# Kernel optimization log

Hardware: AMD Instinct MI355X
Metric: run time of the kernel (lower is better)

## Reference

```python
import jax, jax.numpy as jnp
import numpy as np

N_NODES = 200000
N_EDGES = 6400000
N_LAYERS = 3
Z_DIM = 4  # 2*4 + 1 + 3 == 12 == Linear in_features


def setup_inputs() -> dict:
    key = jax.random.key(0)
    ks = jax.random.split(key, 7)
    z = jax.random.normal(ks[0], (N_NODES, Z_DIM), dtype=jnp.float32)
    r = jax.random.uniform(ks[1], (N_EDGES, 1), dtype=jnp.float32)
    r_hat = jax.random.normal(ks[2], (N_EDGES, 3), dtype=jnp.float32)
    # Per-layer Linear(12, 1) weights and biases, stacked over layers.
    W = jax.random.normal(ks[3], (N_LAYERS, 1, 12), dtype=jnp.float32) * (1.0 / np.sqrt(12.0))
    b = jnp.zeros((N_LAYERS, 1), dtype=jnp.float32)
    src = jax.random.randint(ks[4], (N_EDGES,), 0, N_NODES, dtype=jnp.int32)
    dst = jax.random.randint(ks[5], (N_EDGES,), 0, N_NODES, dtype=jnp.int32)
    return {"z": z, "r": r, "r_hat": r_hat, "W": W, "b": b, "src": src, "dst": dst}


def reference(z, r, r_hat, W, b, src, dst):
    # batch['x'] = batch['z'].copy()
    x = z
    n_nodes = z.shape[0]
    for i in range(W.shape[0]):
        # Per-edge gather + concat -> [E, 12]
        inpt = jnp.concatenate([z[src], z[dst], r, r_hat], axis=-1)
        # Tiny Linear(12, 1) -> per-edge scalar message [E, 1]
        msg = inpt @ W[i].T + b[i]
        # Scatter-sum messages onto destination nodes, residual update.
        agg = jax.ops.segment_sum(msg, dst, num_segments=n_nodes)  # [N, 1]
        z = z + agg  # broadcast over the 4 node features
    return z, x
```

## Files before the change

### kernel.cpp

```cpp
#include <hip/hip_runtime.h>

#define N_NODES 200000
#define N_EDGES 6400000
#define K_BUCKETS 256
#define BUCKET 784
#define NSB 3200
#define CHUNK 2000
#define P_SPLIT 8

__device__ __forceinline__ unsigned short f2bf(float x) {
    unsigned u = __float_as_uint(x);
    u += 0x7fffu + ((u >> 16) & 1u);
    return (unsigned short)(u >> 16);
}
__device__ __forceinline__ float bf2f(unsigned short h) {
    return __uint_as_float((unsigned)h << 16);
}


__global__ __launch_bounds__(256) void prep_kernel(
    const float4* __restrict__ z, float4* __restrict__ x_out,
    const float* __restrict__ W,
    float* __restrict__ u, float* __restrict__ v)
{
    int n = blockIdx.x * 256 + threadIdx.x;
    if (n >= N_NODES) return;
    float4 zv = z[n];
    x_out[n] = zv;
    float a0 = W[0], a1 = W[1], a2 = W[2], a3 = W[3];
    float q0 = W[4], q1 = W[5], q2 = W[6], q3 = W[7];
    u[n] = a0 * zv.x + a1 * zv.y + a2 * zv.z + a3 * zv.w;
    v[n] = q0 * zv.x + q1 * zv.y + q2 * zv.z + q3 * zv.w;
}

__global__ __launch_bounds__(256) void hist_kernel(const int* __restrict__ dst,
                                                   int* __restrict__ counts)
{
    __shared__ int cnt[K_BUCKETS];
    int tid = threadIdx.x, sb = blockIdx.x;
    cnt[tid] = 0;
    __syncthreads();
    int e0 = sb * CHUNK;
    for (int i = tid; i < CHUNK; i += 256)
        atomicAdd(&cnt[dst[e0 + i] / BUCKET], 1);
    __syncthreads();
    counts[sb * K_BUCKETS + tid] = cnt[tid];
}

__global__ __launch_bounds__(256) void scan_cols(const int* __restrict__ counts,
                                                 int* __restrict__ baseRel,
                                                 int* __restrict__ tot)
{
    __shared__ int buf[256];
    __shared__ int carry_s;
    int k = blockIdx.x, tid = threadIdx.x;
    if (tid == 0) carry_s = 0;
    __syncthreads();
    for (int base = 0; base < NSB; base += 256) {
        int idx = base + tid;
        int v = (idx < NSB) ? counts[idx * K_BUCKETS + k] : 0;
        buf[tid] = v;
        __syncthreads();
        for (int off = 1; off < 256; off <<= 1) {
            int t = (tid >= off) ? buf[tid - off] : 0;
            __syncthreads();
            buf[tid] += t;
            __syncthreads();
        }
        int incl = buf[tid];
        if (idx < NSB) baseRel[idx * K_BUCKETS + k] = carry_s + incl - v;
        __syncthreads();
        if (tid == 255) carry_s += incl;
        __syncthreads();
    }
    if (tid == 255) tot[k] = carry_s;
}

__global__ __launch_bounds__(256) void scan_tot(const int* __restrict__ tot,
                                                int* __restrict__ bstart)
{
    __shared__ int buf[256];
    int tid = threadIdx.x;
    int v = tot[tid];
    buf[tid] = v;
    __syncthreads();
    for (int off = 1; off < 256; off <<= 1) {
        int t = (tid >= off) ? buf[tid - off] : 0;
        __syncthreads();
        buf[tid] += t;
        __syncthreads();
    }
    bstart[tid] = buf[tid] - v;
    if (tid == 255) bstart[256] = buf[255];
}

__global__ __launch_bounds__(256) void scatter_kernel(
    const int* __restrict__ src, const int* __restrict__ dst,
    const float* __restrict__ r, const float* __restrict__ r_hat,
    const float* __restrict__ W, const float* __restrict__ b,
    const int* __restrict__ counts, const int* __restrict__ baseRel,
    const int* __restrict__ bstart,
    int* __restrict__ packedA, unsigned* __restrict__ c01a,
    unsigned short* __restrict__ c2a)
{
    __shared__ int cur[K_BUCKETS];
    __shared__ int delta[K_BUCKETS];
    __shared__ int scanbuf[256];
    __shared__ int            lpack[CHUNK];
    __shared__ unsigned       lc01[CHUNK];
    __shared__ unsigned short lc2[CHUNK];
    __shared__ unsigned char  skb[CHUNK];

    int tid = threadIdx.x, sb = blockIdx.x;

    int v = counts[sb * K_BUCKETS + tid];
    scanbuf[tid] = v;
    __syncthreads();
    for (int off = 1; off < 256; off <<= 1) {
        int t = (tid >= off) ? scanbuf[tid - off] : 0;
        __syncthreads();
        scanbuf[tid] += t;
        __syncthreads();
    }
    int localBase = scanbuf[tid] - v;
    int gBase = bstart[tid] + baseRel[sb * K_BUCKETS + tid];
    delta[tid] = gBase - localBase;
    cur[tid] = localBase;
    __syncthreads();

    float w8_0 = W[8],  w9_0 = W[9],  w10_0 = W[10], w11_0 = W[11], b0 = b[0];
    float w8_1 = W[20], w9_1 = W[21], w10_1 = W[22], w11_1 = W[23], b1 = b[1];
    float w8_2 = W[32], w9_2 = W[33], w10_2 = W[34], w11_2 = W[35], b2 = b[2];

    int e0 = sb * CHUNK;
    for (int i = tid; i < CHUNK; i += 256) {
        int e = e0 + i;
        int d = dst[e];
        int k = d / BUCKET;
        int dl = d - k * BUCKET;
        int slot = atomicAdd(&cur[k], 1);
        int sn = src[e];
        float rv = r[e];
        size_t he = 3 * (size_t)e;
        float h0 = r_hat[he], h1 = r_hat[he + 1], h2 = r_hat[he + 2];
        lpack[slot] = (sn << 10) | dl;
        unsigned cc0 = f2bf(w8_0 * rv + w9_0 * h0 + w10_0 * h1 + w11_0 * h2 + b0);
        unsigned cc1 = f2bf(w8_1 * rv + w9_1 * h0 + w10_1 * h1 + w11_1 * h2 + b1);
        lc01[slot] = cc0 | (cc1 << 16);
        lc2[slot]  = f2bf(w8_2 * rv + w9_2 * h0 + w10_2 * h1 + w11_2 * h2 + b2);
        skb[slot]  = (unsigned char)k;
    }
    __syncthreads();

    for (int s = tid; s < CHUNK; s += 256) {
        int k = skb[s];
        int gpos = delta[k] + s;
        packedA[gpos] = lpack[s];
        c01a[gpos] = lc01[s];
        c2a[gpos]  = lc2[s];
    }
}

__global__ __launch_bounds__(256) void pagg_kernel(
    const int* __restrict__ packedA, const unsigned* __restrict__ c01a,
    const unsigned short* __restrict__ c2a, const int* __restrict__ bstart,
    const float* __restrict__ u, const float* __restrict__ v,
    int layer, float* __restrict__ partial)
{
    __shared__ float vsl[BUCKET];
    __shared__ float aggsl[BUCKET];
    int tid = threadIdx.x, blk = blockIdx.x;
    int k = blk / P_SPLIT;
    int p = blk - k * P_SPLIT;
    int nbase = k * BUCKET;
    int nn = min(BUCKET, N_NODES - nbase);

    for (int i = tid; i < BUCKET; i += 256) {
        aggsl[i] = 0.0f;
        vsl[i] = (i < nn) ? v[nbase + i] : 0.0f;
    }
    __syncthreads();

    int estart = bstart[k], eend = bstart[k + 1];
    int len = eend - estart;
    int per = (len + P_SPLIT - 1) / P_SPLIT;
    int lo = estart + p * per;
    int hi = min(lo + per, eend);

    for (int j = lo + tid; j < hi; j += 256) {
        int pack = packedA[j];
        int s = pack >> 10;
        int dl = pack & 1023;
        float c = (layer == 2) ? bf2f(c2a[j])
                               : bf2f((unsigned short)(c01a[j] >> (16 * layer)));
        atomicAdd(&aggsl[dl], u[s] + vsl[dl] + c);
    }
    __syncthreads();

    float* pout = partial + (size_t)blk * BUCKET;
    for (int i = tid; i < BUCKET; i += 256) pout[i] = aggsl[i];
}

__global__ __launch_bounds__(256) void fin_kernel(
    const float4* __restrict__ z0, const float* __restrict__ partial,
    const float* __restrict__ Sin, float* __restrict__ Sout,
    const float* __restrict__ W, int layer,
    float* __restrict__ u, float* __restrict__ v, float4* __restrict__ z_out)
{
    int n = blockIdx.x * 256 + threadIdx.x;
    if (n >= N_NODES) return;
    int k = n / BUCKET;
    int i = n - k * BUCKET;
    float agg = 0.0f;
    const float* pk = partial + (size_t)k * P_SPLIT * BUCKET + i;
#pragma unroll
    for (int p = 0; p < P_SPLIT; ++p) agg += pk[(size_t)p * BUCKET];
    float S = ((layer == 0) ? 0.0f : Sin[n]) + agg;
    if (layer < 2) {
        const float* Wn = W + 12 * (layer + 1);
        float a0 = Wn[0], a1 = Wn[1], a2 = Wn[2], a3 = Wn[3];
        float q0 = Wn[4], q1 = Wn[5], q2 = Wn[6], q3 = Wn[7];
        float A = a0 + a1 + a2 + a3, B = q0 + q1 + q2 + q3;
        float4 zv = z0[n];
        Sout[n] = S;
        u[n] = a0 * zv.x + a1 * zv.y + a2 * zv.z + a3 * zv.w + A * S;
        v[n] = q0 * zv.x + q1 * zv.y + q2 * zv.z + q3 * zv.w + B * S;
    } else {
        float4 zv = z0[n];
        zv.x += S; zv.y += S; zv.z += S; zv.w += S;
        z_out[n] = zv;
    }
}


__global__ __launch_bounds__(256) void init_kernel(
    const float4* __restrict__ z_in, float4* __restrict__ z_cur,
    float4* __restrict__ x_out, float* __restrict__ agg)
{
    int n = blockIdx.x * blockDim.x + threadIdx.x;
    if (n < N_NODES) {
        float4 vv = z_in[n];
        z_cur[n] = vv; x_out[n] = vv; agg[n] = 0.0f;
    }
}

__global__ __launch_bounds__(256) void edge_kernel(
    const float* __restrict__ z, const float* __restrict__ r,
    const float* __restrict__ r_hat, const int* __restrict__ src,
    const int* __restrict__ dst, const float* __restrict__ Wl,
    const float* __restrict__ bl, float* __restrict__ agg)
{
    int e = blockIdx.x * blockDim.x + threadIdx.x;
    if (e >= N_EDGES) return;
    float w0 = Wl[0], w1 = Wl[1], w2 = Wl[2], w3 = Wl[3];
    float w4 = Wl[4], w5 = Wl[5], w6 = Wl[6], w7 = Wl[7];
    float w8 = Wl[8], w9 = Wl[9], w10 = Wl[10], w11 = Wl[11];
    float bias = bl[0];
    int s = src[e], d = dst[e];
    float4 zs = ((const float4*)z)[s];
    float4 zd = ((const float4*)z)[d];
    float rv = r[e];
    const float* rh = r_hat + 3 * (size_t)e;
    float msg = w0*zs.x + w1*zs.y + w2*zs.z + w3*zs.w
              + w4*zd.x + w5*zd.y + w6*zd.z + w7*zd.w
              + w8*rv + w9*rh[0] + w10*rh[1] + w11*rh[2] + bias;
    unsafeAtomicAdd(&agg[d], msg);
}

__global__ __launch_bounds__(256) void node_update(float4* __restrict__ z_cur,
                                                   float* __restrict__ agg)
{
    int n = blockIdx.x * blockDim.x + threadIdx.x;
    if (n < N_NODES) {
        float a = agg[n]; float4 vv = z_cur[n];
        vv.x += a; vv.y += a; vv.z += a; vv.w += a;
        z_cur[n] = vv; agg[n] = 0.0f;
    }
}

__global__ __launch_bounds__(256) void final_update(const float4* __restrict__ z_cur,
                                                    const float* __restrict__ agg,
                                                    float4* __restrict__ z_out)
{
    int n = blockIdx.x * blockDim.x + threadIdx.x;
    if (n < N_NODES) {
        float a = agg[n]; float4 vv = z_cur[n];
        vv.x += a; vv.y += a; vv.z += a; vv.w += a;
        z_out[n] = vv;
    }
}


extern "C" void kernel_launch(void* const* d_in, const int* in_sizes, int n_in,
                              void* d_out, int out_size, void* d_ws, size_t ws_size,
                              hipStream_t stream)
{
    const float* z     = (const float*)d_in[0];
    const float* r     = (const float*)d_in[1];
    const float* r_hat = (const float*)d_in[2];
    const float* W     = (const float*)d_in[3];
    const float* b     = (const float*)d_in[4];
    const int*   src   = (const int*)d_in[5];
    const int*   dst   = (const int*)d_in[6];
    float* out = (float*)d_out;

    char* ws = (char*)d_ws;
    size_t off = 0;
    auto alloc = [&](size_t bytes) {
        void* p = ws + off;
        off += (bytes + 15) & ~(size_t)15;
        return p;
    };
    int*            packedA = (int*)alloc((size_t)N_EDGES * 4);
    unsigned*       c01a    = (unsigned*)alloc((size_t)N_EDGES * 4);
    unsigned short* c2a     = (unsigned short*)alloc((size_t)N_EDGES * 2);
    int*            counts  = (int*)alloc((size_t)NSB * K_BUCKETS * 4);
    int*            baseRel = (int*)alloc((size_t)NSB * K_BUCKETS * 4);
    int*            tot     = (int*)alloc((size_t)K_BUCKETS * 4);
    int*            bstart  = (int*)alloc((size_t)(K_BUCKETS + 1) * 4);
    float*          Sa      = (float*)alloc((size_t)N_NODES * 4);
    float*          Sb      = (float*)alloc((size_t)N_NODES * 4);
    float*          ubuf    = (float*)alloc((size_t)N_NODES * 4);
    float*          vbuf    = (float*)alloc((size_t)N_NODES * 4);
    float*          partial = (float*)alloc((size_t)K_BUCKETS * P_SPLIT * BUCKET * 4);
    size_t required = off;

    dim3 nblk((N_NODES + 255) / 256);

    if (ws_size >= required) {
        prep_kernel<<<nblk, 256, 0, stream>>>(
            (const float4*)z, (float4*)(out + 4 * (size_t)N_NODES), W, ubuf, vbuf);
        hist_kernel<<<NSB, 256, 0, stream>>>(dst, counts);
        scan_cols<<<K_BUCKETS, 256, 0, stream>>>(counts, baseRel, tot);
        scan_tot<<<1, 256, 0, stream>>>(tot, bstart);
        scatter_kernel<<<NSB, 256, 0, stream>>>(src, dst, r, r_hat, W, b,
                                                counts, baseRel, bstart,
                                                packedA, c01a, c2a);
        pagg_kernel<<<K_BUCKETS * P_SPLIT, 256, 0, stream>>>(
            packedA, c01a, c2a, bstart, ubuf, vbuf, 0, partial);
        fin_kernel<<<nblk, 256, 0, stream>>>(
            (const float4*)z, partial, Sa, Sa, W, 0, ubuf, vbuf, (float4*)out);
        pagg_kernel<<<K_BUCKETS * P_SPLIT, 256, 0, stream>>>(
            packedA, c01a, c2a, bstart, ubuf, vbuf, 1, partial);
        fin_kernel<<<nblk, 256, 0, stream>>>(
            (const float4*)z, partial, Sa, Sb, W, 1, ubuf, vbuf, (float4*)out);
        pagg_kernel<<<K_BUCKETS * P_SPLIT, 256, 0, stream>>>(
            packedA, c01a, c2a, bstart, ubuf, vbuf, 2, partial);
        fin_kernel<<<nblk, 256, 0, stream>>>(
            (const float4*)z, partial, Sb, Sb, W, 2, ubuf, vbuf, (float4*)out);
    } else {
        float* agg   = (float*)d_ws;
        float* z_cur = agg + N_NODES;
        dim3 eblk((N_EDGES + 255) / 256);
        init_kernel<<<nblk, 256, 0, stream>>>(
            (const float4*)z, (float4*)z_cur,
            (float4*)(out + 4 * (size_t)N_NODES), agg);
        for (int i = 0; i < 3; ++i) {
            edge_kernel<<<eblk, 256, 0, stream>>>(
                z_cur, r, r_hat, src, dst, W + 12 * i, b + i, agg);
            if (i < 2)
                node_update<<<nblk, 256, 0, stream>>>((float4*)z_cur, agg);
            else
                final_update<<<nblk, 256, 0, stream>>>(
                    (const float4*)z_cur, agg, (float4*)out);
        }
    }
}
```

Baseline: 403.4 us.

## Precompute layer-independent edge sums in one pass, then aggregate only S per layer

```diff
diff --git a/kernel.cpp b/kernel.cpp
--- a/kernel.cpp
+++ b/kernel.cpp
@@ -7,6 +7,7 @@
 #define NSB 3200
 #define CHUNK 2000
 #define P_SPLIT 8
+#define M_SPLIT 2
 
 __device__ __forceinline__ unsigned short f2bf(float x) {
     unsigned u = __float_as_uint(x);
@@ -17,21 +18,6 @@
     return __uint_as_float((unsigned)h << 16);
 }
 
-
-__global__ __launch_bounds__(256) void prep_kernel(
-    const float4* __restrict__ z, float4* __restrict__ x_out,
-    const float* __restrict__ W,
-    float* __restrict__ u, float* __restrict__ v)
-{
-    int n = blockIdx.x * 256 + threadIdx.x;
-    if (n >= N_NODES) return;
-    float4 zv = z[n];
-    x_out[n] = zv;
-    float a0 = W[0], a1 = W[1], a2 = W[2], a3 = W[3];
-    float q0 = W[4], q1 = W[5], q2 = W[6], q3 = W[7];
-    u[n] = a0 * zv.x + a1 * zv.y + a2 * zv.z + a3 * zv.w;
-    v[n] = q0 * zv.x + q1 * zv.y + q2 * zv.z + q3 * zv.w;
-}
 
 __global__ __launch_bounds__(256) void hist_kernel(const int* __restrict__ dst,
                                                    int* __restrict__ counts)
@@ -161,24 +147,94 @@
     }
 }
 
-__global__ __launch_bounds__(256) void pagg_kernel(
+__global__ __launch_bounds__(1024) void magg_kernel(
     const int* __restrict__ packedA, const unsigned* __restrict__ c01a,
     const unsigned short* __restrict__ c2a, const int* __restrict__ bstart,
-    const float* __restrict__ u, const float* __restrict__ v,
-    int layer, float* __restrict__ partial)
-{
-    __shared__ float vsl[BUCKET];
+    const float4* __restrict__ z0, const float* __restrict__ W,
+    float* __restrict__ partial)
+{
+    __shared__ float m0[BUCKET], m1[BUCKET], m2[BUCKET], csl[BUCKET];
+    int tid = threadIdx.x, blk = blockIdx.x;
+    int k = blk >> 1;
+    int p = blk & 1;
+    for (int i = tid; i < BUCKET; i += 1024) {
+        m0[i] = 0.0f; m1[i] = 0.0f; m2[i] = 0.0f; csl[i] = 0.0f;
+    }
+    __syncthreads();
+
+    float a00 = W[0],  a01 = W[1],  a02 = W[2],  a03 = W[3];
+    float a10 = W[12], a11 = W[13], a12 = W[14], a13 = W[15];
+    float a20 = W[24], a21 = W[25], a22 = W[26], a23 = W[27];
+
+    int estart = bstart[k], eend = bstart[k + 1];
+    int len = eend - estart;
+    int per = (len + M_SPLIT - 1) / M_SPLIT;
+    int lo = estart + p * per;
+    int hi = min(lo + per, eend);
+
+    for (int j = lo + tid; j < hi; j += 1024) {
+        int pack = packedA[j];
+        int s = pack >> 10;
+        int dl = pack & 1023;
+        float4 zs = z0[s];
+        unsigned cc = c01a[j];
+        unsigned short c2 = c2a[j];
+        float v0 = a00 * zs.x + a01 * zs.y + a02 * zs.z + a03 * zs.w
+                 + bf2f((unsigned short)(cc & 0xffffu));
+        float v1 = a10 * zs.x + a11 * zs.y + a12 * zs.z + a13 * zs.w
+                 + bf2f((unsigned short)(cc >> 16));
+        float v2 = a20 * zs.x + a21 * zs.y + a22 * zs.z + a23 * zs.w
+                 + bf2f(c2);
+        atomicAdd(&m0[dl], v0);
+        atomicAdd(&m1[dl], v1);
+        atomicAdd(&m2[dl], v2);
+        atomicAdd(&csl[dl], 1.0f);
+    }
+    __syncthreads();
+
+    const size_t AS = (size_t)(M_SPLIT * K_BUCKETS) * BUCKET;
+    float* base = partial + (size_t)blk * BUCKET;
+    for (int i = tid; i < BUCKET; i += 1024) {
+        base[i]          = m0[i];
+        base[AS + i]     = m1[i];
+        base[2 * AS + i] = m2[i];
+        base[3 * AS + i] = csl[i];
+    }
+}
+
+__global__ __launch_bounds__(256) void fin0_kernel(
+    const float4* __restrict__ z0, const float* __restrict__ partial,
+    const float* __restrict__ W,
+    float* __restrict__ S0, float* __restrict__ M1d,
+    float* __restrict__ M2d, float* __restrict__ cntd)
+{
+    int n = blockIdx.x * 256 + threadIdx.x;
+    if (n >= N_NODES) return;
+    int k = n / BUCKET;
+    int i = n - k * BUCKET;
+    const size_t AS = (size_t)(M_SPLIT * K_BUCKETS) * BUCKET;
+    const float* p0 = partial + (size_t)(M_SPLIT * k) * BUCKET + i;
+    float M0 = p0[0]          + p0[BUCKET];
+    float M1 = p0[AS]         + p0[AS + BUCKET];
+    float M2 = p0[2 * AS]     + p0[2 * AS + BUCKET];
+    float C  = p0[3 * AS]     + p0[3 * AS + BUCKET];
+    float4 zv = z0[n];
+    float v0 = W[4] * zv.x + W[5] * zv.y + W[6] * zv.z + W[7] * zv.w;
+    S0[n]   = M0 + C * v0;
+    M1d[n]  = M1;
+    M2d[n]  = M2;
+    cntd[n] = C;
+}
+
+__global__ __launch_bounds__(256) void sagg_kernel(
+    const int* __restrict__ packedA, const int* __restrict__ bstart,
+    const float* __restrict__ S, float* __restrict__ partial)
+{
     __shared__ float aggsl[BUCKET];
     int tid = threadIdx.x, blk = blockIdx.x;
     int k = blk / P_SPLIT;
     int p = blk - k * P_SPLIT;
-    int nbase = k * BUCKET;
-    int nn = min(BUCKET, N_NODES - nbase);
-
-    for (int i = tid; i < BUCKET; i += 256) {
-        aggsl[i] = 0.0f;
-        vsl[i] = (i < nn) ? v[nbase + i] : 0.0f;
-    }
+    for (int i = tid; i < BUCKET; i += 256) aggsl[i] = 0.0f;
     __syncthreads();
 
     int estart = bstart[k], eend = bstart[k + 1];
@@ -189,46 +245,45 @@
 
     for (int j = lo + tid; j < hi; j += 256) {
         int pack = packedA[j];
-        int s = pack >> 10;
-        int dl = pack & 1023;
-        float c = (layer == 2) ? bf2f(c2a[j])
-                               : bf2f((unsigned short)(c01a[j] >> (16 * layer)));
-        atomicAdd(&aggsl[dl], u[s] + vsl[dl] + c);
-    }
-    __syncthreads();
-
-    float* pout = partial + (size_t)blk * BUCKET;
-    for (int i = tid; i < BUCKET; i += 256) pout[i] = aggsl[i];
-}
-
-__global__ __launch_bounds__(256) void fin_kernel(
+        atomicAdd(&aggsl[pack & 1023], S[pack >> 10]);
+    }
+    __syncthreads();
+
+    float* out = partial + (size_t)blk * BUCKET;
+    for (int i = tid; i < BUCKET; i += 256) out[i] = aggsl[i];
+}
+
+__global__ __launch_bounds__(256) void finL_kernel(
     const float4* __restrict__ z0, const float* __restrict__ partial,
-    const float* __restrict__ Sin, float* __restrict__ Sout,
-    const float* __restrict__ W, int layer,
-    float* __restrict__ u, float* __restrict__ v, float4* __restrict__ z_out)
+    const float* __restrict__ Wl,
+    const float* __restrict__ Sprev, const float* __restrict__ Md,
+    const float* __restrict__ cntd, int final_layer,
+    float* __restrict__ Sout, float4* __restrict__ z_out,
+    float4* __restrict__ x_out)
 {
     int n = blockIdx.x * 256 + threadIdx.x;
     if (n >= N_NODES) return;
     int k = n / BUCKET;
     int i = n - k * BUCKET;
-    float agg = 0.0f;
+    float GS = 0.0f;
     const float* pk = partial + (size_t)k * P_SPLIT * BUCKET + i;
 #pragma unroll
-    for (int p = 0; p < P_SPLIT; ++p) agg += pk[(size_t)p * BUCKET];
-    float S = ((layer == 0) ? 0.0f : Sin[n]) + agg;
-    if (layer < 2) {
-        const float* Wn = W + 12 * (layer + 1);
-        float a0 = Wn[0], a1 = Wn[1], a2 = Wn[2], a3 = Wn[3];
-        float q0 = Wn[4], q1 = Wn[5], q2 = Wn[6], q3 = Wn[7];
-        float A = a0 + a1 + a2 + a3, B = q0 + q1 + q2 + q3;
-        float4 zv = z0[n];
+    for (int p = 0; p < P_SPLIT; ++p) GS += pk[(size_t)p * BUCKET];
+
+    float A = Wl[0] + Wl[1] + Wl[2] + Wl[3];
+    float B = Wl[4] + Wl[5] + Wl[6] + Wl[7];
+    float4 zv = z0[n];
+    float vh = Wl[4] * zv.x + Wl[5] * zv.y + Wl[6] * zv.z + Wl[7] * zv.w;
+    float Sp = Sprev[n];
+    float C  = cntd[n];
+    float S  = Sp + Md[n] + A * GS + C * (vh + B * Sp);
+    if (!final_layer) {
         Sout[n] = S;
-        u[n] = a0 * zv.x + a1 * zv.y + a2 * zv.z + a3 * zv.w + A * S;
-        v[n] = q0 * zv.x + q1 * zv.y + q2 * zv.z + q3 * zv.w + B * S;
     } else {
-        float4 zv = z0[n];
+        float4 zo = zv;
         zv.x += S; zv.y += S; zv.z += S; zv.w += S;
         z_out[n] = zv;
+        x_out[n] = zo;
     }
 }
 
@@ -318,36 +373,36 @@
     int*            baseRel = (int*)alloc((size_t)NSB * K_BUCKETS * 4);
     int*            tot     = (int*)alloc((size_t)K_BUCKETS * 4);
     int*            bstart  = (int*)alloc((size_t)(K_BUCKETS + 1) * 4);
-    float*          Sa      = (float*)alloc((size_t)N_NODES * 4);
-    float*          Sb      = (float*)alloc((size_t)N_NODES * 4);
-    float*          ubuf    = (float*)alloc((size_t)N_NODES * 4);
-    float*          vbuf    = (float*)alloc((size_t)N_NODES * 4);
+    float*          S0      = (float*)alloc((size_t)N_NODES * 4);
+    float*          S1M1    = (float*)alloc((size_t)N_NODES * 4);
+    float*          M2d     = (float*)alloc((size_t)N_NODES * 4);
+    float*          cntd    = (float*)alloc((size_t)N_NODES * 4);
     float*          partial = (float*)alloc((size_t)K_BUCKETS * P_SPLIT * BUCKET * 4);
     size_t required = off;
 
     dim3 nblk((N_NODES + 255) / 256);
 
     if (ws_size >= required) {
-        prep_kernel<<<nblk, 256, 0, stream>>>(
-            (const float4*)z, (float4*)(out + 4 * (size_t)N_NODES), W, ubuf, vbuf);
         hist_kernel<<<NSB, 256, 0, stream>>>(dst, counts);
         scan_cols<<<K_BUCKETS, 256, 0, stream>>>(counts, baseRel, tot);
         scan_tot<<<1, 256, 0, stream>>>(tot, bstart);
         scatter_kernel<<<NSB, 256, 0, stream>>>(src, dst, r, r_hat, W, b,
                                                 counts, baseRel, bstart,
                                                 packedA, c01a, c2a);
-        pagg_kernel<<<K_BUCKETS * P_SPLIT, 256, 0, stream>>>(
-            packedA, c01a, c2a, bstart, ubuf, vbuf, 0, partial);
-        fin_kernel<<<nblk, 256, 0, stream>>>(
-            (const float4*)z, partial, Sa, Sa, W, 0, ubuf, vbuf, (float4*)out);
-        pagg_kernel<<<K_BUCKETS * P_SPLIT, 256, 0, stream>>>(
-            packedA, c01a, c2a, bstart, ubuf, vbuf, 1, partial);
-        fin_kernel<<<nblk, 256, 0, stream>>>(
-            (const float4*)z, partial, Sa, Sb, W, 1, ubuf, vbuf, (float4*)out);
-        pagg_kernel<<<K_BUCKETS * P_SPLIT, 256, 0, stream>>>(
-            packedA, c01a, c2a, bstart, ubuf, vbuf, 2, partial);
-        fin_kernel<<<nblk, 256, 0, stream>>>(
-            (const float4*)z, partial, Sb, Sb, W, 2, ubuf, vbuf, (float4*)out);
+        magg_kernel<<<M_SPLIT * K_BUCKETS, 1024, 0, stream>>>(
+            packedA, c01a, c2a, bstart, (const float4*)z, W, partial);
+        fin0_kernel<<<nblk, 256, 0, stream>>>(
+            (const float4*)z, partial, W, S0, S1M1, M2d, cntd);
+        sagg_kernel<<<K_BUCKETS * P_SPLIT, 256, 0, stream>>>(
+            packedA, bstart, S0, partial);
+        finL_kernel<<<nblk, 256, 0, stream>>>(
+            (const float4*)z, partial, W + 12, S0, S1M1, cntd, 0,
+            S1M1, (float4*)out, (float4*)(out + 4 * (size_t)N_NODES));
+        sagg_kernel<<<K_BUCKETS * P_SPLIT, 256, 0, stream>>>(
+            packedA, bstart, S1M1, partial);
+        finL_kernel<<<nblk, 256, 0, stream>>>(
+            (const float4*)z, partial, W + 24, S1M1, M2d, cntd, 1,
+            S0 , (float4*)out, (float4*)(out + 4 * (size_t)N_NODES));
     } else {
         float* agg   = (float*)d_ws;
         float* z_cur = agg + N_NODES;
```

New measurement: 488.9 us. +21.2%, slower.

## Use 64 larger node buckets, 1024-thread aggregation blocks and per-layer coefficient arrays

Applied to the files above, without the earlier changes.

```diff
diff --git a/kernel.cpp b/kernel.cpp
--- a/kernel.cpp
+++ b/kernel.cpp
@@ -2,8 +2,8 @@
 
 #define N_NODES 200000
 #define N_EDGES 6400000
-#define K_BUCKETS 256
-#define BUCKET 784
+#define K_BUCKETS 64
+#define BUCKET 3125
 #define NSB 3200
 #define CHUNK 2000
 #define P_SPLIT 8
@@ -38,13 +38,13 @@
 {
     __shared__ int cnt[K_BUCKETS];
     int tid = threadIdx.x, sb = blockIdx.x;
-    cnt[tid] = 0;
+    if (tid < K_BUCKETS) cnt[tid] = 0;
     __syncthreads();
     int e0 = sb * CHUNK;
     for (int i = tid; i < CHUNK; i += 256)
         atomicAdd(&cnt[dst[e0 + i] / BUCKET], 1);
     __syncthreads();
-    counts[sb * K_BUCKETS + tid] = cnt[tid];
+    if (tid < K_BUCKETS) counts[sb * K_BUCKETS + tid] = cnt[tid];
 }
 
 __global__ __launch_bounds__(256) void scan_cols(const int* __restrict__ counts,
@@ -76,22 +76,22 @@
     if (tid == 255) tot[k] = carry_s;
 }
 
-__global__ __launch_bounds__(256) void scan_tot(const int* __restrict__ tot,
-                                                int* __restrict__ bstart)
-{
-    __shared__ int buf[256];
+__global__ __launch_bounds__(64) void scan_tot(const int* __restrict__ tot,
+                                               int* __restrict__ bstart)
+{
+    __shared__ int buf[K_BUCKETS];
     int tid = threadIdx.x;
     int v = tot[tid];
     buf[tid] = v;
     __syncthreads();
-    for (int off = 1; off < 256; off <<= 1) {
+    for (int off = 1; off < K_BUCKETS; off <<= 1) {
         int t = (tid >= off) ? buf[tid - off] : 0;
         __syncthreads();
         buf[tid] += t;
         __syncthreads();
     }
     bstart[tid] = buf[tid] - v;
-    if (tid == 255) bstart[256] = buf[255];
+    if (tid == K_BUCKETS - 1) bstart[K_BUCKETS] = buf[tid];
 }
 
 __global__ __launch_bounds__(256) void scatter_kernel(
@@ -100,32 +100,39 @@
     const float* __restrict__ W, const float* __restrict__ b,
     const int* __restrict__ counts, const int* __restrict__ baseRel,
     const int* __restrict__ bstart,
-    int* __restrict__ packedA, unsigned* __restrict__ c01a,
-    unsigned short* __restrict__ c2a)
+    int* __restrict__ packedA, unsigned short* __restrict__ c0a,
+    unsigned short* __restrict__ c1a, unsigned short* __restrict__ c2a)
 {
     __shared__ int cur[K_BUCKETS];
     __shared__ int delta[K_BUCKETS];
-    __shared__ int scanbuf[256];
+    __shared__ int scanbuf[K_BUCKETS];
     __shared__ int            lpack[CHUNK];
-    __shared__ unsigned       lc01[CHUNK];
+    __shared__ unsigned short lc0[CHUNK];
+    __shared__ unsigned short lc1[CHUNK];
     __shared__ unsigned short lc2[CHUNK];
     __shared__ unsigned char  skb[CHUNK];
 
     int tid = threadIdx.x, sb = blockIdx.x;
 
-    int v = counts[sb * K_BUCKETS + tid];
-    scanbuf[tid] = v;
-    __syncthreads();
-    for (int off = 1; off < 256; off <<= 1) {
-        int t = (tid >= off) ? scanbuf[tid - off] : 0;
-        __syncthreads();
-        scanbuf[tid] += t;
-        __syncthreads();
-    }
-    int localBase = scanbuf[tid] - v;
-    int gBase = bstart[tid] + baseRel[sb * K_BUCKETS + tid];
-    delta[tid] = gBase - localBase;
-    cur[tid] = localBase;
+    if (tid < K_BUCKETS) {
+        int v = counts[sb * K_BUCKETS + tid];
+        scanbuf[tid] = v;
+    }
+    __syncthreads();
+    for (int off = 1; off < K_BUCKETS; off <<= 1) {
+        int t = 0;
+        if (tid < K_BUCKETS && tid >= off) t = scanbuf[tid - off];
+        __syncthreads();
+        if (tid < K_BUCKETS) scanbuf[tid] += t;
+        __syncthreads();
+    }
+    if (tid < K_BUCKETS) {
+        int v = counts[sb * K_BUCKETS + tid];
+        int localBase = scanbuf[tid] - v;
+        int gBase = bstart[tid] + baseRel[sb * K_BUCKETS + tid];
+        delta[tid] = gBase - localBase;
+        cur[tid] = localBase;
+    }
     __syncthreads();
 
     float w8_0 = W[8],  w9_0 = W[9],  w10_0 = W[10], w11_0 = W[11], b0 = b[0];
@@ -143,12 +150,11 @@
         float rv = r[e];
         size_t he = 3 * (size_t)e;
         float h0 = r_hat[he], h1 = r_hat[he + 1], h2 = r_hat[he + 2];
-        lpack[slot] = (sn << 10) | dl;
-        unsigned cc0 = f2bf(w8_0 * rv + w9_0 * h0 + w10_0 * h1 + w11_0 * h2 + b0);
-        unsigned cc1 = f2bf(w8_1 * rv + w9_1 * h0 + w10_1 * h1 + w11_1 * h2 + b1);
-        lc01[slot] = cc0 | (cc1 << 16);
-        lc2[slot]  = f2bf(w8_2 * rv + w9_2 * h0 + w10_2 * h1 + w11_2 * h2 + b2);
-        skb[slot]  = (unsigned char)k;
+        lpack[slot] = (sn << 12) | dl;
+        lc0[slot] = f2bf(w8_0 * rv + w9_0 * h0 + w10_0 * h1 + w11_0 * h2 + b0);
+        lc1[slot] = f2bf(w8_1 * rv + w9_1 * h0 + w10_1 * h1 + w11_1 * h2 + b1);
+        lc2[slot] = f2bf(w8_2 * rv + w9_2 * h0 + w10_2 * h1 + w11_2 * h2 + b2);
+        skb[slot] = (unsigned char)k;
     }
     __syncthreads();
 
@@ -156,16 +162,17 @@
         int k = skb[s];
         int gpos = delta[k] + s;
         packedA[gpos] = lpack[s];
-        c01a[gpos] = lc01[s];
-        c2a[gpos]  = lc2[s];
-    }
-}
-
-__global__ __launch_bounds__(256) void pagg_kernel(
-    const int* __restrict__ packedA, const unsigned* __restrict__ c01a,
-    const unsigned short* __restrict__ c2a, const int* __restrict__ bstart,
+        c0a[gpos] = lc0[s];
+        c1a[gpos] = lc1[s];
+        c2a[gpos] = lc2[s];
+    }
+}
+
+__global__ __launch_bounds__(1024) void pagg_kernel(
+    const int* __restrict__ packedA, const unsigned short* __restrict__ ca,
+    const int* __restrict__ bstart,
     const float* __restrict__ u, const float* __restrict__ v,
-    int layer, float* __restrict__ partial)
+    float* __restrict__ partial)
 {
     __shared__ float vsl[BUCKET];
     __shared__ float aggsl[BUCKET];
@@ -173,11 +180,10 @@
     int k = blk / P_SPLIT;
     int p = blk - k * P_SPLIT;
     int nbase = k * BUCKET;
-    int nn = min(BUCKET, N_NODES - nbase);
-
-    for (int i = tid; i < BUCKET; i += 256) {
+
+    for (int i = tid; i < BUCKET; i += 1024) {
         aggsl[i] = 0.0f;
-        vsl[i] = (i < nn) ? v[nbase + i] : 0.0f;
+        vsl[i] = v[nbase + i];
     }
     __syncthreads();
 
@@ -187,18 +193,17 @@
     int lo = estart + p * per;
     int hi = min(lo + per, eend);
 
-    for (int j = lo + tid; j < hi; j += 256) {
+    for (int j = lo + tid; j < hi; j += 1024) {
         int pack = packedA[j];
-        int s = pack >> 10;
-        int dl = pack & 1023;
-        float c = (layer == 2) ? bf2f(c2a[j])
-                               : bf2f((unsigned short)(c01a[j] >> (16 * layer)));
-        atomicAdd(&aggsl[dl], u[s] + vsl[dl] + c);
+        int s = pack >> 12;
+        int dl = pack & 4095;
+        float c = bf2f(ca[j]);
+        unsafeAtomicAdd(&aggsl[dl], u[s] + vsl[dl] + c);
     }
     __syncthreads();
 
     float* pout = partial + (size_t)blk * BUCKET;
-    for (int i = tid; i < BUCKET; i += 256) pout[i] = aggsl[i];
+    for (int i = tid; i < BUCKET; i += 1024) pout[i] = aggsl[i];
 }
 
 __global__ __launch_bounds__(256) void fin_kernel(
@@ -312,7 +317,8 @@
         return p;
     };
     int*            packedA = (int*)alloc((size_t)N_EDGES * 4);
-    unsigned*       c01a    = (unsigned*)alloc((size_t)N_EDGES * 4);
+    unsigned short* c0a     = (unsigned short*)alloc((size_t)N_EDGES * 2);
+    unsigned short* c1a     = (unsigned short*)alloc((size_t)N_EDGES * 2);
     unsigned short* c2a     = (unsigned short*)alloc((size_t)N_EDGES * 2);
     int*            counts  = (int*)alloc((size_t)NSB * K_BUCKETS * 4);
     int*            baseRel = (int*)alloc((size_t)NSB * K_BUCKETS * 4);
@@ -332,20 +338,20 @@
             (const float4*)z, (float4*)(out + 4 * (size_t)N_NODES), W, ubuf, vbuf);
         hist_kernel<<<NSB, 256, 0, stream>>>(dst, counts);
         scan_cols<<<K_BUCKETS, 256, 0, stream>>>(counts, baseRel, tot);
-        scan_tot<<<1, 256, 0, stream>>>(tot, bstart);
+        scan_tot<<<1, 64, 0, stream>>>(tot, bstart);
         scatter_kernel<<<NSB, 256, 0, stream>>>(src, dst, r, r_hat, W, b,
                                                 counts, baseRel, bstart,
-                                                packedA, c01a, c2a);
-        pagg_kernel<<<K_BUCKETS * P_SPLIT, 256, 0, stream>>>(
-            packedA, c01a, c2a, bstart, ubuf, vbuf, 0, partial);
+                                                packedA, c0a, c1a, c2a);
+        pagg_kernel<<<K_BUCKETS * P_SPLIT, 1024, 0, stream>>>(
+            packedA, c0a, bstart, ubuf, vbuf, partial);
         fin_kernel<<<nblk, 256, 0, stream>>>(
             (const float4*)z, partial, Sa, Sa, W, 0, ubuf, vbuf, (float4*)out);
-        pagg_kernel<<<K_BUCKETS * P_SPLIT, 256, 0, stream>>>(
-            packedA, c01a, c2a, bstart, ubuf, vbuf, 1, partial);
+        pagg_kernel<<<K_BUCKETS * P_SPLIT, 1024, 0, stream>>>(
+            packedA, c1a, bstart, ubuf, vbuf, partial);
         fin_kernel<<<nblk, 256, 0, stream>>>(
             (const float4*)z, partial, Sa, Sb, W, 1, ubuf, vbuf, (float4*)out);
-        pagg_kernel<<<K_BUCKETS * P_SPLIT, 256, 0, stream>>>(
-            packedA, c01a, c2a, bstart, ubuf, vbuf, 2, partial);
+        pagg_kernel<<<K_BUCKETS * P_SPLIT, 1024, 0, stream>>>(
+            packedA, c2a, bstart, ubuf, vbuf, partial);
         fin_kernel<<<nblk, 256, 0, stream>>>(
             (const float4*)z, partial, Sb, Sb, W, 2, ubuf, vbuf, (float4*)out);
     } else {
```

After: 373.6 us. 1.08x faster.
